# Kernel optimization log

Hardware: AMD Instinct MI355X
Metric: run time of the kernel (lower is better)

The kernel has to match this reference:

```python
import jax, jax.numpy as jnp
import numpy as np

N_HEADS = 16
D_HEAD = 64  # embed_dim // n_heads = 1024 // 16


def setup_inputs() -> dict:
    key = jax.random.key(0)
    ks = jax.random.split(key, 8)
    B, S, E = 2, 2048, 1024
    return {
        "k_in": jax.random.normal(ks[0], (B, S, E), jnp.float32),
        "q_in": jax.random.normal(ks[1], (B, S, E), jnp.float32),
        "v_in": jax.random.normal(ks[2], (B, S, E), jnp.float32),
        "Wq": jax.random.normal(ks[3], (D_HEAD, D_HEAD), jnp.float32) / np.sqrt(D_HEAD),
        "Wk": jax.random.normal(ks[4], (D_HEAD, D_HEAD), jnp.float32) / np.sqrt(D_HEAD),
        "Wv": jax.random.normal(ks[5], (D_HEAD, D_HEAD), jnp.float32) / np.sqrt(D_HEAD),
        "Wo": jax.random.normal(ks[6], (E, E), jnp.float32) / np.sqrt(E),
        "bo": jnp.zeros((E,), jnp.float32),
    }


def reference(k_in, q_in, v_in, Wq, Wk, Wv, Wo, bo):
    B, Sq, E = q_in.shape
    Sk = k_in.shape[1]
    H, Dh = N_HEADS, D_HEAD
    # split heads: [B, S, H, Dh]
    q = q_in.reshape(B, Sq, H, Dh)
    k = k_in.reshape(B, Sk, H, Dh)
    v = v_in.reshape(B, Sk, H, Dh)
    # per-head linear projections (nn.Linear: x @ W.T), then [B, H, S, Dh]
    q = jnp.einsum("bshd,ed->bhse", q, Wq)
    k = jnp.einsum("bshd,ed->bhse", k, Wk)
    v = jnp.einsum("bshd,ed->bhse", v, Wv)
    # scaled dot-product attention
    scores = jnp.einsum("bhqd,bhkd->bhqk", q, k) / jnp.sqrt(jnp.asarray(Dh, q.dtype))
    attn = jax.nn.softmax(scores, axis=-1)
    ctx = jnp.einsum("bhqk,bhkd->bqhd", attn, v)  # [B, Sq, H, Dh]
    concat = ctx.reshape(B, Sq, H * Dh)
    return concat @ Wo.T + bo
```

## Files before the change

### kernel.cpp

```cpp
#include <hip/hip_runtime.h>
#include <hip/hip_fp16.h>

typedef _Float16 f16;
typedef __fp16 hf16x2 __attribute__((ext_vector_type(2)));
typedef _Float16 f16x8 __attribute__((ext_vector_type(8)));
typedef _Float16 f16x4v __attribute__((ext_vector_type(4)));
typedef float f32x4 __attribute__((ext_vector_type(4)));

#define B_ 2
#define S_ 2048
#define E_ 1024
#define H_ 16
#define DH_ 64

__device__ __forceinline__ f32x4 mfma16(f16x8 a, f16x8 b, f32x4 c) {
    return __builtin_amdgcn_mfma_f32_16x16x32_f16(a, b, c, 0, 0, 0);
}

__device__ __forceinline__ f32x4 vmax4(f32x4 a, f32x4 b) {
    f32x4 r;
    r[0] = fmaxf(a[0], b[0]); r[1] = fmaxf(a[1], b[1]);
    r[2] = fmaxf(a[2], b[2]); r[3] = fmaxf(a[3], b[3]);
    return r;
}

__device__ __forceinline__ f16x8 cvt8(const float* p) {
    float4 v0 = *(const float4*)p;
    float4 v1 = *(const float4*)(p + 4);
    f16x8 r;
    r[0] = (f16)v0.x; r[1] = (f16)v0.y; r[2] = (f16)v0.z; r[3] = (f16)v0.w;
    r[4] = (f16)v1.x; r[5] = (f16)v1.y; r[6] = (f16)v1.z; r[7] = (f16)v1.w;
    return r;
}

__global__ __launch_bounds__(256) void proj_cvt_kernel(
    const float* __restrict__ q_in, const float* __restrict__ k_in,
    const float* __restrict__ v_in,
    const float* __restrict__ Wq, const float* __restrict__ Wk,
    const float* __restrict__ Wv, const float* __restrict__ Wo,
    f16* __restrict__ Qg, f16* __restrict__ Kg, f16* __restrict__ Vt,
    f16* __restrict__ WoH)
{
    int tid = threadIdx.x;
    int bx = blockIdx.x;
    if (bx >= 3072) {
        int i = (bx - 3072) * 256 + tid;
        float4 v = *(const float4*)(Wo + (size_t)i * 4);
        f16x4v o;
        o[0] = (f16)v.x; o[1] = (f16)v.y; o[2] = (f16)v.z; o[3] = (f16)v.w;
        *(f16x4v*)(WoH + (size_t)i * 4) = o;
        return;
    }

    int lane = tid & 63, wv = tid >> 6;
    int wid = bx * 4 + wv;
    int proj = wid >> 12;
    int r = wid & 4095;
    int bh = r >> 7;
    int stile = r & 127;
    int sbase = stile * 16;
    int h = bh & 15;
    int b = bh >> 4;
    int c = lane & 15, g = lane >> 4;

    const float* x; const float* W;
    if (proj == 0)      { x = q_in; W = Wq; }
    else if (proj == 1) { x = k_in; W = Wk; }
    else                { x = v_in; W = Wv; }

    const float* xrow = x + (((size_t)(b * S_ + sbase + c) * H_ + h) << 6);
    f16x8 a0 = cvt8(xrow + g * 8);
    f16x8 a1 = cvt8(xrow + 32 + g * 8);

    f32x4 acc[4] = {};
#pragma unroll
    for (int nt = 0; nt < 4; ++nt) {
        const float* wrow = W + ((nt * 16 + c) << 6);
        f16x8 b0 = cvt8(wrow + g * 8);
        f16x8 b1 = cvt8(wrow + 32 + g * 8);
        acc[nt] = mfma16(a0, b0, acc[nt]);
        acc[nt] = mfma16(a1, b1, acc[nt]);
    }

    if (proj < 2) {
        f16* out = (proj == 0) ? Qg : Kg;
#pragma unroll
        for (int nt = 0; nt < 4; ++nt)
#pragma unroll
            for (int j = 0; j < 4; ++j) {
                int s = sbase + g * 4 + j;
                out[((size_t)bh * S_ + s) * DH_ + nt * 16 + c] = (f16)acc[nt][j];
            }
    } else {
#pragma unroll
        for (int nt = 0; nt < 4; ++nt) {
            f16x4v pk;
            pk[0] = (f16)acc[nt][0]; pk[1] = (f16)acc[nt][1];
            pk[2] = (f16)acc[nt][2]; pk[3] = (f16)acc[nt][3];
            *(f16x4v*)&Vt[((size_t)bh * DH_ + nt * 16 + c) * S_ + sbase + g * 4] = pk;
        }
    }
}

#define C1_ 0.18033688011112042f

__global__ __launch_bounds__(256, 4) void attn_kernel(
    const f16* __restrict__ Qg, const f16* __restrict__ Kg,
    const f16* __restrict__ Vt, f16* __restrict__ ctx)
{
    __shared__ __align__(16) f16 Kl[2][64 * 64];
    __shared__ __align__(16) f16 Vl[2][64 * 64];
    __shared__ __align__(16) f16 Pl[4][16 * 64];

    int tid = threadIdx.x, lane = tid & 63, wv = tid >> 6;
    int bid = blockIdx.x;
    int sb = (bid & 7) * 128 + (bid >> 3);
    int bh = sb >> 5, qt = sb & 31;
    int b = bh >> 4, h = bh & 15;
    int qbase = qt * 64 + wv * 16;
    int c = lane & 15, g = lane >> 4;
    int swz = (c & 7) << 3;

    const f16* Qh = Qg + (size_t)bh * S_ * DH_;
    const f16* Kh = Kg + (size_t)bh * S_ * DH_;
    const f16* Vh = Vt + (size_t)bh * DH_ * S_;

    int s0 = tid, s1 = tid + 256;
    int kr0 = s0 >> 3, kc0 = s0 & 7, kr1 = s1 >> 3, kc1 = s1 & 7;
    int kd0 = kr0 * 64 + ((kc0 * 8) ^ ((kr0 & 7) << 3));
    int kd1 = kr1 * 64 + ((kc1 * 8) ^ ((kr1 & 7) << 3));
    const f16* ksp0 = Kh + kr0 * 64 + kc0 * 8;
    const f16* ksp1 = Kh + kr1 * 64 + kc1 * 8;
    const f16* vsp0 = Vh + kr0 * S_ + kc0 * 8;
    const f16* vsp1 = Vh + kr1 * S_ + kc1 * 8;

    f16x8 qf[2];
#pragma unroll
    for (int hh = 0; hh < 2; ++hh)
        qf[hh] = *(const f16x8*)(Qh + (size_t)(qbase + c) * DH_ + hh * 32 + g * 8);

    float m2 = -1e30f;
    f32x4 lrv = {};
    f32x4 accO[4] = {};
    f16x8 kreg0, kreg1, vreg0, vreg1;

    kreg0 = *(const f16x8*)ksp0; kreg1 = *(const f16x8*)ksp1;
    vreg0 = *(const f16x8*)vsp0; vreg1 = *(const f16x8*)vsp1;
    *(f16x8*)&Kl[0][kd0] = kreg0; *(f16x8*)&Kl[0][kd1] = kreg1;
    *(f16x8*)&Vl[0][kd0] = vreg0; *(f16x8*)&Vl[0][kd1] = vreg1;
    __syncthreads();

#define ATTN_STEP(CUR, T, STAGE)                                               \
    do {                                                                       \
        if (STAGE) {                                                           \
            int ko = ((T) + 1) * 64 * 64, vo = ((T) + 1) * 64;                 \
            kreg0 = *(const f16x8*)(ksp0 + ko);                                \
            kreg1 = *(const f16x8*)(ksp1 + ko);                                \
            vreg0 = *(const f16x8*)(vsp0 + vo);                                \
            vreg1 = *(const f16x8*)(vsp1 + vo);                                \
        }                                                                      \
        f32x4 accS[4] = {};                                                    \
        __builtin_amdgcn_s_setprio(1);                                         \
        _Pragma("unroll")                                                      \
        for (int ks = 0; ks < 4; ++ks) {                                       \
            int krow = (ks * 16 + c) * 64;                                     \
            f16x8 k0 = *(const f16x8*)&Kl[CUR][krow + ((8 * g) ^ swz)];        \
            f16x8 k1 = *(const f16x8*)&Kl[CUR][krow + ((32 + 8 * g) ^ swz)];   \
            accS[ks] = mfma16(k0, qf[0], accS[ks]);                            \
            accS[ks] = mfma16(k1, qf[1], accS[ks]);                            \
        }                                                                      \
        __builtin_amdgcn_s_setprio(0);                                         \
        f32x4 mx4 = vmax4(vmax4(accS[0], accS[1]), vmax4(accS[2], accS[3]));   \
        float rmax = fmaxf(fmaxf(mx4[0], mx4[1]), fmaxf(mx4[2], mx4[3]));      \
        if (!__all(fmaf(rmax, C1_, -m2) <= 8.f)) {                             \
            float mx = fmaxf(rmax, __shfl_xor(rmax, 16));                      \
            mx = fmaxf(mx, __shfl_xor(mx, 32));                                \
            float mn = fmaxf(m2, mx * C1_);                                    \
            float al = exp2f(m2 - mn);                                         \
            m2 = mn;                                                           \
            _Pragma("unroll")                                                  \
            for (int j = 0; j < 4; ++j) lrv[j] *= al;                          \
            _Pragma("unroll")                                                  \
            for (int j = 0; j < 4; ++j) {                                      \
                float aj = __shfl(al, 4 * g + j);                              \
                _Pragma("unroll")                                              \
                for (int nt = 0; nt < 4; ++nt) accO[nt][j] *= aj;              \
            }                                                                  \
        }                                                                      \
        _Pragma("unroll")                                                      \
        for (int ks = 0; ks < 4; ++ks) {                                       \
            f32x4 e;                                                           \
            _Pragma("unroll")                                                  \
            for (int j = 0; j < 4; ++j)                                        \
                e[j] = exp2f(fmaf(accS[ks][j], C1_, -m2));                     \
            lrv += e;                                                          \
            hf16x2 lo = __builtin_amdgcn_cvt_pkrtz(e[0], e[1]);                \
            hf16x2 hi = __builtin_amdgcn_cvt_pkrtz(e[2], e[3]);                \
            uint2 w;                                                           \
            w.x = __builtin_bit_cast(unsigned, lo);                            \
            w.y = __builtin_bit_cast(unsigned, hi);                            \
            *(uint2*)&Pl[wv][c * 64 + ((16 * ks + 4 * g) ^ swz)] = w;          \
        }                                                                      \
        __builtin_amdgcn_s_setprio(1);                                         \
        _Pragma("unroll")                                                      \
        for (int kh = 0; kh < 2; ++kh) {                                       \
            f16x8 pa = *(const f16x8*)&Pl[wv][c * 64 + ((32 * kh + 8 * g) ^ swz)];\
            _Pragma("unroll")                                                  \
            for (int nt = 0; nt < 4; ++nt) {                                   \
                f16x8 vb = *(const f16x8*)&Vl[CUR][(nt * 16 + c) * 64          \
                                + ((32 * kh + 8 * g) ^ swz)];                  \
                accO[nt] = mfma16(pa, vb, accO[nt]);                           \
            }                                                                  \
        }                                                                      \
        __builtin_amdgcn_s_setprio(0);                                         \
        if (STAGE) {                                                           \
            int nb = (CUR) ^ 1;                                                \
            *(f16x8*)&Kl[nb][kd0] = kreg0; *(f16x8*)&Kl[nb][kd1] = kreg1;      \
            *(f16x8*)&Vl[nb][kd0] = vreg0; *(f16x8*)&Vl[nb][kd1] = vreg1;      \
            __syncthreads();                                                   \
        }                                                                      \
    } while (0)

#pragma unroll 1
    for (int kt = 0; kt < 30; kt += 2) {
        ATTN_STEP(0, kt, 1);
        ATTN_STEP(1, kt + 1, 1);
    }
    ATTN_STEP(0, 30, 1);
    ATTN_STEP(1, 31, 0);
#undef ATTN_STEP

    float lr = (lrv[0] + lrv[1]) + (lrv[2] + lrv[3]);
    lr += __shfl_xor(lr, 16);
    lr += __shfl_xor(lr, 32);
    float inv = 1.f / lr;
#pragma unroll
    for (int j = 0; j < 4; ++j) {
        float lj = __shfl(inv, 4 * g + j);
        int s = qbase + 4 * g + j;
#pragma unroll
        for (int nt = 0; nt < 4; ++nt)
            ctx[((size_t)b * S_ + s) * E_ + h * DH_ + nt * 16 + c] =
                (f16)(accO[nt][j] * lj);
    }
}

__global__ __launch_bounds__(256) void gemm_out(
    const f16* __restrict__ A,
    const f16* __restrict__ Bw,
    const float* __restrict__ bo,
    float* __restrict__ out)
{
    __shared__ __align__(16) f16 Al[2][128 * 64];
    __shared__ __align__(16) f16 Bl[2][64 * 64];

    int tid = threadIdx.x, lane = tid & 63, wv = tid >> 6;
    int bid = blockIdx.x;
    int sb = (bid & 7) * 64 + (bid >> 3);
    int mbase = (sb & 31) * 128, nbase = (sb >> 5) * 64;
    int c = lane & 15, g = lane >> 4;
    int wr = wv >> 1, wc = wv & 1;
    int swz = (c & 7) << 3;

    int adst[4]; const f16* asrc[4];
#pragma unroll
    for (int i = 0; i < 4; ++i) {
        int slot = tid + i * 256;
        int row = slot >> 3, cc = slot & 7;
        adst[i] = row * 64 + ((cc * 8) ^ ((row & 7) << 3));
        asrc[i] = A + (size_t)(mbase + row) * 1024 + cc * 8;
    }
    int bdst[2]; const f16* bsrc[2];
#pragma unroll
    for (int i = 0; i < 2; ++i) {
        int slot = tid + i * 256;
        int row = slot >> 3, cc = slot & 7;
        bdst[i] = row * 64 + ((cc * 8) ^ ((row & 7) << 3));
        bsrc[i] = Bw + (size_t)(nbase + row) * 1024 + cc * 8;
    }

    f32x4 acc[4][2] = {};
    f16x8 areg[4], breg[2];

#pragma unroll
    for (int i = 0; i < 4; ++i) areg[i] = *(const f16x8*)asrc[i];
#pragma unroll
    for (int i = 0; i < 2; ++i) breg[i] = *(const f16x8*)bsrc[i];
#pragma unroll
    for (int i = 0; i < 4; ++i) *(f16x8*)&Al[0][adst[i]] = areg[i];
#pragma unroll
    for (int i = 0; i < 2; ++i) *(f16x8*)&Bl[0][bdst[i]] = breg[i];
    __syncthreads();

#define GEMM_STEP(CUR, T, STAGE)                                               \
    do {                                                                       \
        if (STAGE) {                                                           \
            _Pragma("unroll")                                                  \
            for (int i = 0; i < 4; ++i)                                        \
                areg[i] = *(const f16x8*)(asrc[i] + ((T) + 1) * 64);           \
            _Pragma("unroll")                                                  \
            for (int i = 0; i < 2; ++i)                                        \
                breg[i] = *(const f16x8*)(bsrc[i] + ((T) + 1) * 64);           \
        }                                                                      \
        __builtin_amdgcn_s_setprio(1);                                         \
        _Pragma("unroll")                                                      \
        for (int kk = 0; kk < 2; ++kk) {                                       \
            f16x8 af[4], bf[2];                                                \
            _Pragma("unroll")                                                  \
            for (int mi = 0; mi < 4; ++mi)                                     \
                af[mi] = *(const f16x8*)&Al[CUR][(wr * 64 + mi * 16 + c) * 64  \
                                               + ((32 * kk + 8 * g) ^ swz)];   \
            _Pragma("unroll")                                                  \
            for (int ni = 0; ni < 2; ++ni)                                     \
                bf[ni] = *(const f16x8*)&Bl[CUR][(wc * 32 + ni * 16 + c) * 64  \
                                               + ((32 * kk + 8 * g) ^ swz)];   \
            _Pragma("unroll")                                                  \
            for (int mi = 0; mi < 4; ++mi)                                     \
                _Pragma("unroll")                                              \
                for (int ni = 0; ni < 2; ++ni)                                 \
                    acc[mi][ni] = mfma16(af[mi], bf[ni], acc[mi][ni]);         \
        }                                                                      \
        __builtin_amdgcn_s_setprio(0);                                         \
        if (STAGE) {                                                           \
            int nb = (CUR) ^ 1;                                                \
            _Pragma("unroll")                                                  \
            for (int i = 0; i < 4; ++i) *(f16x8*)&Al[nb][adst[i]] = areg[i];   \
            _Pragma("unroll")                                                  \
            for (int i = 0; i < 2; ++i) *(f16x8*)&Bl[nb][bdst[i]] = breg[i];   \
            __syncthreads();                                                   \
        }                                                                      \
    } while (0)

#pragma unroll 1
    for (int ks = 0; ks < 14; ks += 2) {
        GEMM_STEP(0, ks, 1);
        GEMM_STEP(1, ks + 1, 1);
    }
    GEMM_STEP(0, 14, 1);
    GEMM_STEP(1, 15, 0);
#undef GEMM_STEP

#pragma unroll
    for (int ni = 0; ni < 2; ++ni) {
        float bias = bo[nbase + wc * 32 + ni * 16 + c];
#pragma unroll
        for (int mi = 0; mi < 4; ++mi)
#pragma unroll
            for (int j = 0; j < 4; ++j) {
                int m = mbase + wr * 64 + mi * 16 + g * 4 + j;
                out[(size_t)m * 1024 + nbase + wc * 32 + ni * 16 + c] =
                    acc[mi][ni][j] + bias;
            }
    }
}

extern "C" void kernel_launch(void* const* d_in, const int* in_sizes, int n_in,
                              void* d_out, int out_size, void* d_ws, size_t ws_size,
                              hipStream_t stream)
{
    const float* k_in = (const float*)d_in[0];
    const float* q_in = (const float*)d_in[1];
    const float* v_in = (const float*)d_in[2];
    const float* Wq   = (const float*)d_in[3];
    const float* Wk   = (const float*)d_in[4];
    const float* Wv   = (const float*)d_in[5];
    const float* Wo   = (const float*)d_in[6];
    const float* bo   = (const float*)d_in[7];
    float* out = (float*)d_out;

    char* ws = (char*)d_ws;
    f16* Qg  = (f16*)(ws);
    f16* Kg  = (f16*)(ws + (8u << 20));
    f16* Vt  = (f16*)(ws + (16u << 20));
    f16* ctx = (f16*)(ws + (24u << 20));
    f16* WoH = (f16*)(ws + (32u << 20));

    proj_cvt_kernel<<<dim3(4096), dim3(256), 0, stream>>>(
        q_in, k_in, v_in, Wq, Wk, Wv, Wo, Qg, Kg, Vt, WoH);
    attn_kernel<<<dim3(1024), dim3(256), 0, stream>>>(Qg, Kg, Vt, ctx);
    gemm_out<<<dim3(512), dim3(256), 0, stream>>>(ctx, WoH, bo, out);
}
```

Before: 120.5 us.

## Switch attention to 32x32 MFMA tiles with register-shuffled P operand

The attention kernel moves from 16x16x32 to 32x32x16 MFMA. Each wave now owns 32 query rows, so a block covers 128 queries and the grid is halved. The softmax probabilities are passed to the PV matmul through cross-lane shuffles instead of a round trip through a shared-memory P buffer. K and V tiles sit in a single swizzled LDS array with a new layout. This cuts LDS traffic and synchronisation and reuses each loaded K/V tile across more queries, but it raises register pressure (launch bounds drop to 2 blocks per SM) and leaves fewer blocks to fill the GPU.

```diff
diff --git a/kernel.cpp b/kernel.cpp
--- a/kernel.cpp
+++ b/kernel.cpp
@@ -6,6 +6,7 @@
 typedef _Float16 f16x8 __attribute__((ext_vector_type(8)));
 typedef _Float16 f16x4v __attribute__((ext_vector_type(4)));
 typedef float f32x4 __attribute__((ext_vector_type(4)));
+typedef float f32x16 __attribute__((ext_vector_type(16)));
 
 #define B_ 2
 #define S_ 2048
@@ -16,12 +17,8 @@
 __device__ __forceinline__ f32x4 mfma16(f16x8 a, f16x8 b, f32x4 c) {
     return __builtin_amdgcn_mfma_f32_16x16x32_f16(a, b, c, 0, 0, 0);
 }
-
-__device__ __forceinline__ f32x4 vmax4(f32x4 a, f32x4 b) {
-    f32x4 r;
-    r[0] = fmaxf(a[0], b[0]); r[1] = fmaxf(a[1], b[1]);
-    r[2] = fmaxf(a[2], b[2]); r[3] = fmaxf(a[3], b[3]);
-    return r;
+__device__ __forceinline__ f32x16 mfma32(f16x8 a, f16x8 b, f32x16 c) {
+    return __builtin_amdgcn_mfma_f32_32x32x16_f16(a, b, c, 0, 0, 0);
 }
 
 __device__ __forceinline__ f16x8 cvt8(const float* p) {
@@ -104,119 +101,135 @@
 
 #define C1_ 0.18033688011112042f
 
-__global__ __launch_bounds__(256, 4) void attn_kernel(
+__global__ __launch_bounds__(256, 2) void attn_kernel(
     const f16* __restrict__ Qg, const f16* __restrict__ Kg,
     const f16* __restrict__ Vt, f16* __restrict__ ctx)
 {
-    __shared__ __align__(16) f16 Kl[2][64 * 64];
-    __shared__ __align__(16) f16 Vl[2][64 * 64];
-    __shared__ __align__(16) f16 Pl[4][16 * 64];
+    __shared__ __align__(16) f16 lds[16384];
 
     int tid = threadIdx.x, lane = tid & 63, wv = tid >> 6;
     int bid = blockIdx.x;
-    int sb = (bid & 7) * 128 + (bid >> 3);
-    int bh = sb >> 5, qt = sb & 31;
+    int sb = (bid & 7) * 64 + (bid >> 3);
+    int bh = sb >> 4, qt = sb & 15;
     int b = bh >> 4, h = bh & 15;
-    int qbase = qt * 64 + wv * 16;
-    int c = lane & 15, g = lane >> 4;
-    int swz = (c & 7) << 3;
+    int qbase = qt * 128 + wv * 32;
+    int q32 = lane & 31, hh = lane >> 5;
+    bool isLo = (hh == 0);
 
     const f16* Qh = Qg + (size_t)bh * S_ * DH_;
     const f16* Kh = Kg + (size_t)bh * S_ * DH_;
     const f16* Vh = Vt + (size_t)bh * DH_ * S_;
 
+    int swzr = (q32 & 15) << 3;
+    int cr[8];
+#pragma unroll
+    for (int a = 0; a < 2; ++a)
+#pragma unroll
+        for (int s = 0; s < 4; ++s)
+            cr[4 * a + s] = q32 * 128 + ((a * 64 + 16 * s + 8 * hh) ^ swzr);
+
     int s0 = tid, s1 = tid + 256;
-    int kr0 = s0 >> 3, kc0 = s0 & 7, kr1 = s1 >> 3, kc1 = s1 & 7;
-    int kd0 = kr0 * 64 + ((kc0 * 8) ^ ((kr0 & 7) << 3));
-    int kd1 = kr1 * 64 + ((kc1 * 8) ^ ((kr1 & 7) << 3));
-    const f16* ksp0 = Kh + kr0 * 64 + kc0 * 8;
-    const f16* ksp1 = Kh + kr1 * 64 + kc1 * 8;
-    const f16* vsp0 = Vh + kr0 * S_ + kc0 * 8;
-    const f16* vsp1 = Vh + kr1 * S_ + kc1 * 8;
-
-    f16x8 qf[2];
-#pragma unroll
-    for (int hh = 0; hh < 2; ++hh)
-        qf[hh] = *(const f16x8*)(Qh + (size_t)(qbase + c) * DH_ + hh * 32 + g * 8);
-
-    float m2 = -1e30f;
-    f32x4 lrv = {};
-    f32x4 accO[4] = {};
+    int e0 = s0 >> 3, c0 = s0 & 7, e1 = s1 >> 3, c1 = s1 & 7;
+    int wd0 = (e0 & 31) * 128 + ((((e0 >> 5) * 64) + c0 * 8) ^ (((e0 & 31) & 15) << 3));
+    int wd1 = (e1 & 31) * 128 + ((((e1 >> 5) * 64) + c1 * 8) ^ (((e1 & 31) & 15) << 3));
+    const f16* ksp0 = Kh + e0 * 64 + c0 * 8;
+    const f16* ksp1 = Kh + e1 * 64 + c1 * 8;
+    const f16* vsp0 = Vh + (size_t)e0 * S_ + c0 * 8;
+    const f16* vsp1 = Vh + (size_t)e1 * S_ + c1 * 8;
+
+    f16x8 qf[4];
+#pragma unroll
+    for (int s = 0; s < 4; ++s)
+        qf[s] = *(const f16x8*)(Qh + (size_t)(qbase + q32) * DH_ + 16 * s + 8 * hh);
+
+    float m2 = -1e30f, lrv = 0.f;
+    f32x16 accO0 = {}, accO1 = {};
     f16x8 kreg0, kreg1, vreg0, vreg1;
 
     kreg0 = *(const f16x8*)ksp0; kreg1 = *(const f16x8*)ksp1;
     vreg0 = *(const f16x8*)vsp0; vreg1 = *(const f16x8*)vsp1;
-    *(f16x8*)&Kl[0][kd0] = kreg0; *(f16x8*)&Kl[0][kd1] = kreg1;
-    *(f16x8*)&Vl[0][kd0] = vreg0; *(f16x8*)&Vl[0][kd1] = vreg1;
+    *(f16x8*)&lds[wd0] = kreg0; *(f16x8*)&lds[wd1] = kreg1;
+    *(f16x8*)&lds[8192 + wd0] = vreg0; *(f16x8*)&lds[8192 + wd1] = vreg1;
     __syncthreads();
+
+#define ATTN_SUB(CUR, SUBI)                                                    \
+    do {                                                                       \
+        f32x16 accS = {};                                                      \
+        __builtin_amdgcn_s_setprio(1);                                         \
+        _Pragma("unroll")                                                      \
+        for (int s = 0; s < 4; ++s) {                                          \
+            f16x8 kf = *(const f16x8*)&lds[(CUR) * 4096 + cr[4 * (SUBI) + s]]; \
+            accS = mfma32(kf, qf[s], accS);                                    \
+        }                                                                      \
+        __builtin_amdgcn_s_setprio(0);                                         \
+        float rmax = accS[0];                                                  \
+        _Pragma("unroll")                                                      \
+        for (int r = 1; r < 16; ++r) rmax = fmaxf(rmax, accS[r]);              \
+        rmax = fmaxf(rmax, __shfl_xor(rmax, 32));                              \
+        if (!__all(fmaf(rmax, C1_, -m2) <= 8.f)) {                             \
+            float mn = fmaxf(m2, rmax * C1_);                                  \
+            float al = exp2f(m2 - mn);                                         \
+            m2 = mn; lrv *= al;                                                \
+            _Pragma("unroll")                                                  \
+            for (int r = 0; r < 16; ++r) {                                     \
+                float aj = __shfl(al, ((r & 3) + 8 * (r >> 2)) + 4 * hh);      \
+                accO0[r] *= aj; accO1[r] *= aj;                                \
+            }                                                                  \
+        }                                                                      \
+        unsigned w[8];                                                         \
+        _Pragma("unroll")                                                      \
+        for (int j = 0; j < 8; ++j) {                                          \
+            float ea = exp2f(fmaf(accS[2 * j], C1_, -m2));                     \
+            float eb = exp2f(fmaf(accS[2 * j + 1], C1_, -m2));                 \
+            lrv += ea + eb;                                                    \
+            hf16x2 pk = __builtin_amdgcn_cvt_pkrtz(ea, eb);                    \
+            w[j] = __builtin_bit_cast(unsigned, pk);                           \
+        }                                                                      \
+        _Pragma("unroll")                                                      \
+        for (int s2 = 0; s2 < 2; ++s2) {                                       \
+            unsigned b0 = w[4 * s2 + 0], b1 = w[4 * s2 + 1];                   \
+            unsigned b2 = w[4 * s2 + 2], b3 = w[4 * s2 + 3];                   \
+            unsigned x0 = (unsigned)__shfl_xor((int)b0, 32);                   \
+            unsigned x1 = (unsigned)__shfl_xor((int)b1, 32);                   \
+            unsigned x2 = (unsigned)__shfl_xor((int)b2, 32);                   \
+            unsigned x3 = (unsigned)__shfl_xor((int)b3, 32);                   \
+            uint4 au;                                                          \
+            au.x = isLo ? b0 : x2;                                             \
+            au.y = isLo ? b1 : x3;                                             \
+            au.z = isLo ? x0 : b2;                                             \
+            au.w = isLo ? x1 : b3;                                             \
+            f16x8 pa = __builtin_bit_cast(f16x8, au);                          \
+            __builtin_amdgcn_s_setprio(1);                                     \
+            {                                                                  \
+                f16x8 vb = *(const f16x8*)&lds[8192 + (CUR) * 4096             \
+                                               + cr[(SUBI) * 2 + s2]];         \
+                accO0 = mfma32(pa, vb, accO0);                                 \
+            }                                                                  \
+            {                                                                  \
+                f16x8 vb = *(const f16x8*)&lds[8192 + (CUR) * 4096             \
+                                               + cr[4 + (SUBI) * 2 + s2]];     \
+                accO1 = mfma32(pa, vb, accO1);                                 \
+            }                                                                  \
+            __builtin_amdgcn_s_setprio(0);                                     \
+        }                                                                      \
+    } while (0)
 
 #define ATTN_STEP(CUR, T, STAGE)                                               \
     do {                                                                       \
         if (STAGE) {                                                           \
-            int ko = ((T) + 1) * 64 * 64, vo = ((T) + 1) * 64;                 \
-            kreg0 = *(const f16x8*)(ksp0 + ko);                                \
-            kreg1 = *(const f16x8*)(ksp1 + ko);                                \
-            vreg0 = *(const f16x8*)(vsp0 + vo);                                \
-            vreg1 = *(const f16x8*)(vsp1 + vo);                                \
-        }                                                                      \
-        f32x4 accS[4] = {};                                                    \
-        __builtin_amdgcn_s_setprio(1);                                         \
-        _Pragma("unroll")                                                      \
-        for (int ks = 0; ks < 4; ++ks) {                                       \
-            int krow = (ks * 16 + c) * 64;                                     \
-            f16x8 k0 = *(const f16x8*)&Kl[CUR][krow + ((8 * g) ^ swz)];        \
-            f16x8 k1 = *(const f16x8*)&Kl[CUR][krow + ((32 + 8 * g) ^ swz)];   \
-            accS[ks] = mfma16(k0, qf[0], accS[ks]);                            \
-            accS[ks] = mfma16(k1, qf[1], accS[ks]);                            \
-        }                                                                      \
-        __builtin_amdgcn_s_setprio(0);                                         \
-        f32x4 mx4 = vmax4(vmax4(accS[0], accS[1]), vmax4(accS[2], accS[3]));   \
-        float rmax = fmaxf(fmaxf(mx4[0], mx4[1]), fmaxf(mx4[2], mx4[3]));      \
-        if (!__all(fmaf(rmax, C1_, -m2) <= 8.f)) {                             \
-            float mx = fmaxf(rmax, __shfl_xor(rmax, 16));                      \
-            mx = fmaxf(mx, __shfl_xor(mx, 32));                                \
-            float mn = fmaxf(m2, mx * C1_);                                    \
-            float al = exp2f(m2 - mn);                                         \
-            m2 = mn;                                                           \
-            _Pragma("unroll")                                                  \
-            for (int j = 0; j < 4; ++j) lrv[j] *= al;                          \
-            _Pragma("unroll")                                                  \
-            for (int j = 0; j < 4; ++j) {                                      \
-                float aj = __shfl(al, 4 * g + j);                              \
-                _Pragma("unroll")                                              \
-                for (int nt = 0; nt < 4; ++nt) accO[nt][j] *= aj;              \
-            }                                                                  \
-        }                                                                      \
-        _Pragma("unroll")                                                      \
-        for (int ks = 0; ks < 4; ++ks) {                                       \
-            f32x4 e;                                                           \
-            _Pragma("unroll")                                                  \
-            for (int j = 0; j < 4; ++j)                                        \
-                e[j] = exp2f(fmaf(accS[ks][j], C1_, -m2));                     \
-            lrv += e;                                                          \
-            hf16x2 lo = __builtin_amdgcn_cvt_pkrtz(e[0], e[1]);                \
-            hf16x2 hi = __builtin_amdgcn_cvt_pkrtz(e[2], e[3]);                \
-            uint2 w;                                                           \
-            w.x = __builtin_bit_cast(unsigned, lo);                            \
-            w.y = __builtin_bit_cast(unsigned, hi);                            \
-            *(uint2*)&Pl[wv][c * 64 + ((16 * ks + 4 * g) ^ swz)] = w;          \
-        }                                                                      \
-        __builtin_amdgcn_s_setprio(1);                                         \
-        _Pragma("unroll")                                                      \
-        for (int kh = 0; kh < 2; ++kh) {                                       \
-            f16x8 pa = *(const f16x8*)&Pl[wv][c * 64 + ((32 * kh + 8 * g) ^ swz)];\
-            _Pragma("unroll")                                                  \
-            for (int nt = 0; nt < 4; ++nt) {                                   \
-                f16x8 vb = *(const f16x8*)&Vl[CUR][(nt * 16 + c) * 64          \
-                                + ((32 * kh + 8 * g) ^ swz)];                  \
-                accO[nt] = mfma16(pa, vb, accO[nt]);                           \
-            }                                                                  \
-        }                                                                      \
-        __builtin_amdgcn_s_setprio(0);                                         \
+            kreg0 = *(const f16x8*)(ksp0 + ((T) + 1) * 4096);                  \
+            kreg1 = *(const f16x8*)(ksp1 + ((T) + 1) * 4096);                  \
+            vreg0 = *(const f16x8*)(vsp0 + ((T) + 1) * 64);                    \
+            vreg1 = *(const f16x8*)(vsp1 + ((T) + 1) * 64);                    \
+        }                                                                      \
+        ATTN_SUB(CUR, 0);                                                      \
+        ATTN_SUB(CUR, 1);                                                      \
         if (STAGE) {                                                           \
             int nb = (CUR) ^ 1;                                                \
-            *(f16x8*)&Kl[nb][kd0] = kreg0; *(f16x8*)&Kl[nb][kd1] = kreg1;      \
-            *(f16x8*)&Vl[nb][kd0] = vreg0; *(f16x8*)&Vl[nb][kd1] = vreg1;      \
+            *(f16x8*)&lds[nb * 4096 + wd0] = kreg0;                            \
+            *(f16x8*)&lds[nb * 4096 + wd1] = kreg1;                            \
+            *(f16x8*)&lds[8192 + nb * 4096 + wd0] = vreg0;                     \
+            *(f16x8*)&lds[8192 + nb * 4096 + wd1] = vreg1;                     \
             __syncthreads();                                                   \
         }                                                                      \
     } while (0)
@@ -229,19 +242,18 @@
     ATTN_STEP(0, 30, 1);
     ATTN_STEP(1, 31, 0);
 #undef ATTN_STEP
-
-    float lr = (lrv[0] + lrv[1]) + (lrv[2] + lrv[3]);
-    lr += __shfl_xor(lr, 16);
-    lr += __shfl_xor(lr, 32);
+#undef ATTN_SUB
+
+    float lr = lrv + __shfl_xor(lrv, 32);
     float inv = 1.f / lr;
 #pragma unroll
-    for (int j = 0; j < 4; ++j) {
-        float lj = __shfl(inv, 4 * g + j);
-        int s = qbase + 4 * g + j;
-#pragma unroll
-        for (int nt = 0; nt < 4; ++nt)
-            ctx[((size_t)b * S_ + s) * E_ + h * DH_ + nt * 16 + c] =
-                (f16)(accO[nt][j] * lj);
+    for (int r = 0; r < 16; ++r) {
+        int crow = (r & 3) + 8 * (r >> 2);
+        float ir = __shfl(inv, crow + 4 * hh);
+        int s = qbase + crow + 4 * hh;
+        f16* dst = ctx + ((size_t)b * S_ + s) * E_ + h * DH_ + q32;
+        dst[0]  = (f16)(accO0[r] * ir);
+        dst[32] = (f16)(accO1[r] * ir);
     }
 }
 
@@ -377,6 +389,6 @@
 
     proj_cvt_kernel<<<dim3(4096), dim3(256), 0, stream>>>(
         q_in, k_in, v_in, Wq, Wk, Wv, Wo, Qg, Kg, Vt, WoH);
-    attn_kernel<<<dim3(1024), dim3(256), 0, stream>>>(Qg, Kg, Vt, ctx);
+    attn_kernel<<<dim3(512), dim3(256), 0, stream>>>(Qg, Kg, Vt, ctx);
     gemm_out<<<dim3(512), dim3(256), 0, stream>>>(ctx, WoH, bo, out);
 }
```

Result: no change. 118.6 us (-1.5%).
